# Performance work log

Measured on AMD Instinct MI355X. Metric: run time of the kernel, lower is better.

The kernel has to match this reference:

```python
import jax, jax.numpy as jnp
import numpy as np

B, T, IN_DIM = 128, 4096, 13
UNITS, MOTOR = 64, 6
LAYERS = [35, 23, 6]   # AutoNCP(64, 6): inter / command / motor neurons
_SPLITS = [35, 58]     # cumulative layer boundaries inside the 64-unit state


def setup_inputs() -> dict:
    keys = iter(jax.random.split(jax.random.key(0), 64))
    def rn(shape, s=0.1):
        return jax.random.normal(next(keys), shape, dtype=jnp.float32) * s
    inp = {"x": jax.random.normal(next(keys), (B, T, IN_DIM), dtype=jnp.float32)}
    # mixed-memory LSTM cell (ncps: input_map has bias, recurrent_map does not)
    inp["lstm_wi"] = rn((4 * UNITS, IN_DIM))
    inp["lstm_wh"] = rn((4 * UNITS, UNITS))
    inp["lstm_b"] = rn((4 * UNITS,))
    # wired CfC layers: ff1/ff2/time_a/time_b acting on concat([input, h])
    in_dims = [IN_DIM] + LAYERS[:-1]
    for i, (d, h) in enumerate(zip(in_dims, LAYERS)):
        for nm in ("w1", "w2", "wa", "wb"):
            inp[f"cfc{i}_{nm}"] = rn((h, d + h))
        for nm in ("b1", "b2", "ba", "bb"):
            inp[f"cfc{i}_{nm}"] = rn((h,))
    inp["gyro_w1"] = rn((32, MOTOR)); inp["gyro_b1"] = rn((32,))
    inp["gyro_w2"] = rn((3, 32));     inp["gyro_b2"] = rn((3,))
    inp["acc_w1"] = rn((32, MOTOR));  inp["acc_b1"] = rn((32,))
    inp["acc_w2"] = rn((3, 32));      inp["acc_b2"] = rn((3,))
    inp["unc_w1"] = rn((16, MOTOR));  inp["unc_b1"] = rn((16,))
    inp["unc_w2"] = rn((6, 16));      inp["unc_b2"] = rn((6,))
    return inp


def _cfc_step(inp, h, p):
    """ncps CfCCell, mode='default', no backbone, ts = 1.0."""
    W1, b1, W2, b2, Wa, ba, Wb, bb = p
    z = jnp.concatenate([inp, h], axis=-1)            # (B, in+hid)
    ff1 = jnp.tanh(z @ W1.T + b1)
    ff2 = jnp.tanh(z @ W2.T + b2)
    t = jax.nn.sigmoid((z @ Wa.T + ba) + (z @ Wb.T + bb))  # t_a*ts + t_b, ts==1
    return ff1 * (1.0 - t) + t * ff2


def reference(x, lstm_wi, lstm_wh, lstm_b,
              cfc0_w1, cfc0_b1, cfc0_w2, cfc0_b2, cfc0_wa, cfc0_ba, cfc0_wb, cfc0_bb,
              cfc1_w1, cfc1_b1, cfc1_w2, cfc1_b2, cfc1_wa, cfc1_ba, cfc1_wb, cfc1_bb,
              cfc2_w1, cfc2_b1, cfc2_w2, cfc2_b2, cfc2_wa, cfc2_ba, cfc2_wb, cfc2_bb,
              gyro_w1, gyro_b1, gyro_w2, gyro_b2,
              acc_w1, acc_b1, acc_w2, acc_b2,
              unc_w1, unc_b1, unc_w2, unc_b2):
    layer_params = (
        (cfc0_w1, cfc0_b1, cfc0_w2, cfc0_b2, cfc0_wa, cfc0_ba, cfc0_wb, cfc0_bb),
        (cfc1_w1, cfc1_b1, cfc1_w2, cfc1_b2, cfc1_wa, cfc1_ba, cfc1_wb, cfc1_bb),
        (cfc2_w1, cfc2_b1, cfc2_w2, cfc2_b2, cfc2_wa, cfc2_ba, cfc2_wb, cfc2_bb),
    )

    def step(carry, xt):  # xt: (B, 13)
        h, c = carry
        # mixed-memory LSTM over the full 64-unit state (forget gate +1.0)
        zg = xt @ lstm_wi.T + lstm_b + h @ lstm_wh.T
        ia, ig, fg, og = jnp.split(zg, 4, axis=-1)
        c_new = c * jax.nn.sigmoid(fg + 1.0) + jnp.tanh(ia) * jax.nn.sigmoid(ig)
        h_lstm = jnp.tanh(c_new) * jax.nn.sigmoid(og)
        # wired CfC: inter -> command -> motor, each fed previous layer's output
        hs = jnp.split(h_lstm, _SPLITS, axis=-1)
        inp = xt
        new_hs = []
        for hi, p in zip(hs, layer_params):
            inp = _cfc_step(inp, hi, p)
            new_hs.append(inp)
        return (jnp.concatenate(new_hs, axis=-1), c_new), inp  # motor out (B,6)

    Bsz = x.shape[0]
    h0 = jnp.zeros((Bsz, UNITS), x.dtype)
    c0 = jnp.zeros((Bsz, UNITS), x.dtype)
    _, outs = jax.lax.scan(step, (h0, c0), jnp.swapaxes(x, 0, 1))
    cfc_out = jnp.swapaxes(outs, 0, 1)  # (B, T, 6)

    gyro = jnp.tanh(cfc_out @ gyro_w1.T + gyro_b1) @ gyro_w2.T + gyro_b2
    acc = jnp.tanh(cfc_out @ acc_w1.T + acc_b1) @ acc_w2.T + acc_b2
    pred = jnp.concatenate([gyro, acc], axis=-1)                      # (B, T, 6)
    unc = jax.nn.softplus(
        jax.nn.relu(cfc_out @ unc_w1.T + unc_b1) @ unc_w2.T + unc_b2)  # (B, T, 6)
    return pred, unc
```

## Files before the change

### kernel.cpp

```cpp
#include <hip/hip_runtime.h>
#include <math.h>

#define BATCH 128
#define TSTEPS 4096
#define INDIM 13
#define XT 64


__device__ __forceinline__ float fsig(float x) {
    return __builtin_amdgcn_rcpf(1.f + __expf(-x));
}
__device__ __forceinline__ float ftanh(float x) {
    float s = fsig(x + x);
    return s + s - 1.f;
}
__device__ __forceinline__ float fsoftplus(float x) {
    return (x > 15.f) ? x : __logf(1.f + __expf(x));
}

__device__ __forceinline__ float qxor1(float v) {
    return __int_as_float(__builtin_amdgcn_update_dpp(
        0, __float_as_int(v), 0xB1, 0xF, 0xF, true));
}
__device__ __forceinline__ float qxor2(float v) {
    return __int_as_float(__builtin_amdgcn_update_dpp(
        0, __float_as_int(v), 0x4E, 0xF, 0xF, true));
}
__device__ __forceinline__ float hmir(float v) {
    return __int_as_float(__builtin_amdgcn_update_dpp(
        0, __float_as_int(v), 0x141, 0xF, 0xF, true));
}
#define BFLY8(a) { a += qxor1(a); a += qxor2(a); a += hmir(a); }

#define FMA4(acc, W, q, zv) { acc += zv.x * W##_##q##_0; acc += zv.y * W##_##q##_1; \
                              acc += zv.z * W##_##q##_2; acc += zv.w * W##_##q##_3; }

__global__ __launch_bounds__(512, 2)
void rnn_kernel(const float* __restrict__ x,
                const float* __restrict__ lstm_wi, const float* __restrict__ lstm_wh,
                const float* __restrict__ lstm_b,
                const float* __restrict__ c0w1, const float* __restrict__ c0w2,
                const float* __restrict__ c0wa, const float* __restrict__ c0wb,
                const float* __restrict__ c0b1, const float* __restrict__ c0b2,
                const float* __restrict__ c0ba, const float* __restrict__ c0bb,
                const float* __restrict__ c1w1, const float* __restrict__ c1w2,
                const float* __restrict__ c1wa, const float* __restrict__ c1wb,
                const float* __restrict__ c1b1, const float* __restrict__ c1b2,
                const float* __restrict__ c1ba, const float* __restrict__ c1bb,
                const float* __restrict__ c2w1, const float* __restrict__ c2w2,
                const float* __restrict__ c2wa, const float* __restrict__ c2wb,
                const float* __restrict__ c2b1, const float* __restrict__ c2b2,
                const float* __restrict__ c2ba, const float* __restrict__ c2bb,
                float* __restrict__ out)
{
    const int bb = blockIdx.x;
    const int t  = threadIdx.x;
    const int k  = t & 7;
    const int u  = t >> 3;

    __shared__ __align__(16) float smem[2688];
    float* zL  = smem;
    float* z0  = smem + 96;
    float* z1  = smem + 160;
    float* z2  = smem + 224;
    float* xt0 = smem + 256;
    float* xt1 = smem + 1088;
    float* ot0 = smem + 1920;
    float* ot1 = smem + 2304;

    const long xbase = (long)bb * TSTEPS * INDIM;
    const long obase = (long)bb * TSTEPS * 6;

    auto lwf = [&](int A, int c) -> float {
        int r = A * 64 + u;
        return (c < 13) ? lstm_wi[r * 13 + c]
             : (c < 77) ? lstm_wh[r * 64 + (c - 13)] : 0.f;
    };
#define DEF_WL(A,q) \
    float wl##A##_##q##_0 = lwf(A, 12*k + 4*q + 0); \
    float wl##A##_##q##_1 = lwf(A, 12*k + 4*q + 1); \
    float wl##A##_##q##_2 = lwf(A, 12*k + 4*q + 2); \
    float wl##A##_##q##_3 = lwf(A, 12*k + 4*q + 3);
    DEF_WL(0,0) DEF_WL(0,1) DEF_WL(0,2)
    DEF_WL(1,0) DEF_WL(1,1) DEF_WL(1,2)
    DEF_WL(2,0) DEF_WL(2,1) DEF_WL(2,2)
    DEF_WL(3,0) DEF_WL(3,1) DEF_WL(3,2)
#undef DEF_WL
    const float bL0 = lstm_b[u];
    const float bL1 = lstm_b[64 + u];
    const float bL2 = lstm_b[128 + u];
    const float bL3 = lstm_b[192 + u];

    const int grp  = (u < 35) ? 0 : (u < 58) ? 1 : 2;
    const int row  = (grp == 0) ? u : (grp == 1) ? (u - 35) : (u - 58);
    const int rl   = (grp == 0) ? 48 : (grp == 1) ? 58 : 29;
    const int clen = (grp == 2) ? 4 : 8;
    const int cb   = (grp == 2) ? 4 * k : 8 * k;
    const float *W0p, *W1p, *W2p, *W3p;
    float bC0, bC1, bC2, bC3;
    if (grp == 0) {
        W0p = c0w1 + row * 48; W1p = c0w2 + row * 48;
        W2p = c0wa + row * 48; W3p = c0wb + row * 48;
        bC0 = c0b1[row]; bC1 = c0b2[row]; bC2 = c0ba[row]; bC3 = c0bb[row];
    } else if (grp == 1) {
        W0p = c1w1 + row * 58; W1p = c1w2 + row * 58;
        W2p = c1wa + row * 58; W3p = c1wb + row * 58;
        bC0 = c1b1[row]; bC1 = c1b2[row]; bC2 = c1ba[row]; bC3 = c1bb[row];
    } else {
        W0p = c2w1 + row * 29; W1p = c2w2 + row * 29;
        W2p = c2wa + row * 29; W3p = c2wb + row * 29;
        bC0 = c2b1[row]; bC1 = c2b2[row]; bC2 = c2ba[row]; bC3 = c2bb[row];
    }
    auto cwf = [&](const float* W, int c) -> float {
        int cc = cb + c;
        return (c < clen && cc < rl) ? W[cc] : 0.f;
    };
#define DEF_WC(A,q) \
    float wc##A##_##q##_0 = cwf(W##A##p, 4*q + 0); \
    float wc##A##_##q##_1 = cwf(W##A##p, 4*q + 1); \
    float wc##A##_##q##_2 = cwf(W##A##p, 4*q + 2); \
    float wc##A##_##q##_3 = cwf(W##A##p, 4*q + 3);
    DEF_WC(0,0) DEF_WC(0,1)
    DEF_WC(1,0) DEF_WC(1,1)
    DEF_WC(2,0) DEF_WC(2,1)
    DEF_WC(3,0) DEF_WC(3,1)
#undef DEF_WC

    float creg = 0.f;

    if (t < 256) smem[t] = 0.f;
    if (t < 208) {
        float4 xi = *(const float4*)(x + xbase + 4 * t);
        *(float4*)&xt0[4 * t] = xi;
    }
    if (t < 13) zL[t] = x[xbase + t];
    __syncthreads();

    #pragma unroll 1
    for (int ts = 0; ts < TSTEPS; ++ts) {
        const int par = (ts >> 6) & 1;
        const int lts = ts & 63;

        if (t >= 256 && t < 269) z0[t - 256] = zL[t - 256];
        {
            const float4* zc = (const float4*)(zL + 12 * k);
            float4 q0 = zc[0], q1 = zc[1], q2 = zc[2];
            float a0 = 0.f, a1 = 0.f, a2 = 0.f, a3 = 0.f;
            FMA4(a0, wl0, 0, q0) FMA4(a0, wl0, 1, q1) FMA4(a0, wl0, 2, q2)
            FMA4(a1, wl1, 0, q0) FMA4(a1, wl1, 1, q1) FMA4(a1, wl1, 2, q2)
            FMA4(a2, wl2, 0, q0) FMA4(a2, wl2, 1, q1) FMA4(a2, wl2, 2, q2)
            FMA4(a3, wl3, 0, q0) FMA4(a3, wl3, 1, q1) FMA4(a3, wl3, 2, q2)
            BFLY8(a0) BFLY8(a1) BFLY8(a2) BFLY8(a3)
            a0 += bL0; a1 += bL1; a2 += bL2; a3 += bL3;
            float cn = creg * fsig(a2 + 1.f) + ftanh(a0) * fsig(a1);
            creg = cn;
            float hl = ftanh(cn) * fsig(a3);
            if (k == 0) {
                if (u < 35)      z0[13 + u] = hl;
                else if (u < 58) z1[u]      = hl;
                else             z2[u - 35] = hl;
            }
        }
        __syncthreads();

        if (grp == 0) {
            const float4* zc = (const float4*)(z0 + 8 * k);
            float4 v0 = zc[0], v1 = zc[1];
            float a0 = 0.f, a1 = 0.f, a2 = 0.f, a3 = 0.f;
            FMA4(a0, wc0, 0, v0) FMA4(a0, wc0, 1, v1)
            FMA4(a1, wc1, 0, v0) FMA4(a1, wc1, 1, v1)
            FMA4(a2, wc2, 0, v0) FMA4(a2, wc2, 1, v1)
            FMA4(a3, wc3, 0, v0) FMA4(a3, wc3, 1, v1)
            BFLY8(a0) BFLY8(a1) BFLY8(a2) BFLY8(a3)
            a0 += bC0; a1 += bC1; a2 += bC2; a3 += bC3;
            float tg = fsig(a2 + a3);
            float f1 = ftanh(a0), f2 = ftanh(a1);
            float o = f1 + tg * (f2 - f1);
            if (k == 0) { z1[row] = o; zL[13 + row] = o; }
        } else {
            if (lts == 62 && (ts + 2) < TSTEPS) {
                int i = t - 280;
                if (i < 208) {
                    float4 v = *(const float4*)(x + xbase + (long)(ts + 2) * 13 + 4 * i);
                    float* dst = par ? xt0 : xt1;
                    *(float4*)&dst[4 * i] = v;
                }
            }
            if (lts == 0 && ts > 0) {
                int i = t - 280;
                if (i < 96) {
                    const float* src = par ? ot0 : ot1;
                    float4 v = *(const float4*)&src[4 * i];
                    *(float4*)(out + obase + (long)(ts - XT) * 6 + 4 * i) = v;
                }
            }
        }
        __syncthreads();

        if (grp == 1) {
            const float4* zc = (const float4*)(z1 + 8 * k);
            float4 v0 = zc[0], v1 = zc[1];
            float a0 = 0.f, a1 = 0.f, a2 = 0.f, a3 = 0.f;
            FMA4(a0, wc0, 0, v0) FMA4(a0, wc0, 1, v1)
            FMA4(a1, wc1, 0, v0) FMA4(a1, wc1, 1, v1)
            FMA4(a2, wc2, 0, v0) FMA4(a2, wc2, 1, v1)
            FMA4(a3, wc3, 0, v0) FMA4(a3, wc3, 1, v1)
            BFLY8(a0) BFLY8(a1) BFLY8(a2) BFLY8(a3)
            a0 += bC0; a1 += bC1; a2 += bC2; a3 += bC3;
            float tg = fsig(a2 + a3);
            float f1 = ftanh(a0), f2 = ftanh(a1);
            float o = f1 + tg * (f2 - f1);
            if (k == 0) { z2[row] = o; zL[48 + row] = o; }
        }
        __syncthreads();

        if (grp == 2) {
            const float4* zc = (const float4*)(z2 + 4 * k);
            float4 v0 = zc[0];
            float a0 = 0.f, a1 = 0.f, a2 = 0.f, a3 = 0.f;
            FMA4(a0, wc0, 0, v0)
            FMA4(a1, wc1, 0, v0)
            FMA4(a2, wc2, 0, v0)
            FMA4(a3, wc3, 0, v0)
            BFLY8(a0) BFLY8(a1) BFLY8(a2) BFLY8(a3)
            a0 += bC0; a1 += bC1; a2 += bC2; a3 += bC3;
            float tg = fsig(a2 + a3);
            float f1 = ftanh(a0), f2 = ftanh(a1);
            float o = f1 + tg * (f2 - f1);
            if (k == 0) {
                zL[71 + row] = o;
                float* ob = par ? ot1 : ot0;
                ob[lts * 6 + row] = o;
            }
        } else if (t < 13 && (ts + 1) < TSTEPS) {
            const float* xb = (((ts + 1) >> 6) & 1) ? xt1 : xt0;
            zL[t] = xb[((ts + 1) & 63) * 13 + t];
        }
        __syncthreads();
    }

    {
        int i = t - 280;
        if (i >= 0 && i < 96) {
            float4 v = *(const float4*)&ot1[4 * i];
            *(float4*)(out + obase + (long)(TSTEPS - XT) * 6 + 4 * i) = v;
        }
    }
}

#define S_GW1 0
#define S_GB1 192
#define S_GW2 224
#define S_GB2 320
#define S_AW1 323
#define S_AB1 515
#define S_AW2 547
#define S_AB2 643
#define S_UW1 646
#define S_UB1 742
#define S_UW2 758
#define S_UB2 854
#define S_TOT 860

__global__ __launch_bounds__(256)
void head_kernel(const float* __restrict__ gw1, const float* __restrict__ gb1,
                 const float* __restrict__ gw2, const float* __restrict__ gb2,
                 const float* __restrict__ aw1, const float* __restrict__ ab1,
                 const float* __restrict__ aw2, const float* __restrict__ ab2,
                 const float* __restrict__ uw1, const float* __restrict__ ub1,
                 const float* __restrict__ uw2, const float* __restrict__ ub2,
                 float* __restrict__ out)
{
    __shared__ float s[S_TOT];
    const int t = threadIdx.x;
    if (t < 192) { s[S_GW1 + t] = gw1[t]; s[S_AW1 + t] = aw1[t]; }
    if (t < 96)  { s[S_GW2 + t] = gw2[t]; s[S_AW2 + t] = aw2[t];
                   s[S_UW1 + t] = uw1[t]; s[S_UW2 + t] = uw2[t]; }
    if (t < 32)  { s[S_GB1 + t] = gb1[t]; s[S_AB1 + t] = ab1[t]; }
    if (t < 16)  { s[S_UB1 + t] = ub1[t]; }
    if (t < 3)   { s[S_GB2 + t] = gb2[t]; s[S_AB2 + t] = ab2[t]; }
    if (t < 6)   { s[S_UB2 + t] = ub2[t]; }
    __syncthreads();

    const long p = (long)blockIdx.x * 256 + t;
    const long base = p * 6;
    float m0 = out[base+0], m1 = out[base+1], m2 = out[base+2];
    float m3 = out[base+3], m4 = out[base+4], m5 = out[base+5];

    float gy0 = s[S_GB2+0], gy1 = s[S_GB2+1], gy2 = s[S_GB2+2];
    float ac0 = s[S_AB2+0], ac1 = s[S_AB2+1], ac2 = s[S_AB2+2];
    #pragma unroll
    for (int i = 0; i < 32; ++i) {
        float hg = s[S_GB1+i] + s[S_GW1+i*6+0]*m0 + s[S_GW1+i*6+1]*m1
                 + s[S_GW1+i*6+2]*m2 + s[S_GW1+i*6+3]*m3
                 + s[S_GW1+i*6+4]*m4 + s[S_GW1+i*6+5]*m5;
        hg = ftanh(hg);
        gy0 += s[S_GW2+i]*hg; gy1 += s[S_GW2+32+i]*hg; gy2 += s[S_GW2+64+i]*hg;
        float ha = s[S_AB1+i] + s[S_AW1+i*6+0]*m0 + s[S_AW1+i*6+1]*m1
                 + s[S_AW1+i*6+2]*m2 + s[S_AW1+i*6+3]*m3
                 + s[S_AW1+i*6+4]*m4 + s[S_AW1+i*6+5]*m5;
        ha = ftanh(ha);
        ac0 += s[S_AW2+i]*ha; ac1 += s[S_AW2+32+i]*ha; ac2 += s[S_AW2+64+i]*ha;
    }
    float u0 = s[S_UB2+0], u1 = s[S_UB2+1], u2 = s[S_UB2+2];
    float u3 = s[S_UB2+3], u4 = s[S_UB2+4], u5 = s[S_UB2+5];
    #pragma unroll
    for (int i = 0; i < 16; ++i) {
        float hu = s[S_UB1+i] + s[S_UW1+i*6+0]*m0 + s[S_UW1+i*6+1]*m1
                 + s[S_UW1+i*6+2]*m2 + s[S_UW1+i*6+3]*m3
                 + s[S_UW1+i*6+4]*m4 + s[S_UW1+i*6+5]*m5;
        hu = fmaxf(hu, 0.f);
        u0 += s[S_UW2+i]*hu;      u1 += s[S_UW2+16+i]*hu; u2 += s[S_UW2+32+i]*hu;
        u3 += s[S_UW2+48+i]*hu;   u4 += s[S_UW2+64+i]*hu; u5 += s[S_UW2+80+i]*hu;
    }
    out[base+0] = gy0; out[base+1] = gy1; out[base+2] = gy2;
    out[base+3] = ac0; out[base+4] = ac1; out[base+5] = ac2;
    const long uoff = (long)BATCH * TSTEPS * 6;
    out[uoff+base+0] = fsoftplus(u0); out[uoff+base+1] = fsoftplus(u1);
    out[uoff+base+2] = fsoftplus(u2); out[uoff+base+3] = fsoftplus(u3);
    out[uoff+base+4] = fsoftplus(u4); out[uoff+base+5] = fsoftplus(u5);
}

extern "C" void kernel_launch(void* const* d_in, const int* in_sizes, int n_in,
                              void* d_out, int out_size, void* d_ws, size_t ws_size,
                              hipStream_t stream) {
    const float* x       = (const float*)d_in[0];
    const float* lstm_wi = (const float*)d_in[1];
    const float* lstm_wh = (const float*)d_in[2];
    const float* lstm_b  = (const float*)d_in[3];
    const float* c0w1 = (const float*)d_in[4];
    const float* c0w2 = (const float*)d_in[5];
    const float* c0wa = (const float*)d_in[6];
    const float* c0wb = (const float*)d_in[7];
    const float* c0b1 = (const float*)d_in[8];
    const float* c0b2 = (const float*)d_in[9];
    const float* c0ba = (const float*)d_in[10];
    const float* c0bb = (const float*)d_in[11];
    const float* c1w1 = (const float*)d_in[12];
    const float* c1w2 = (const float*)d_in[13];
    const float* c1wa = (const float*)d_in[14];
    const float* c1wb = (const float*)d_in[15];
    const float* c1b1 = (const float*)d_in[16];
    const float* c1b2 = (const float*)d_in[17];
    const float* c1ba = (const float*)d_in[18];
    const float* c1bb = (const float*)d_in[19];
    const float* c2w1 = (const float*)d_in[20];
    const float* c2w2 = (const float*)d_in[21];
    const float* c2wa = (const float*)d_in[22];
    const float* c2wb = (const float*)d_in[23];
    const float* c2b1 = (const float*)d_in[24];
    const float* c2b2 = (const float*)d_in[25];
    const float* c2ba = (const float*)d_in[26];
    const float* c2bb = (const float*)d_in[27];
    const float* gw1 = (const float*)d_in[28];
    const float* gb1 = (const float*)d_in[29];
    const float* gw2 = (const float*)d_in[30];
    const float* gb2 = (const float*)d_in[31];
    const float* aw1 = (const float*)d_in[32];
    const float* ab1 = (const float*)d_in[33];
    const float* aw2 = (const float*)d_in[34];
    const float* ab2 = (const float*)d_in[35];
    const float* uw1 = (const float*)d_in[36];
    const float* ub1 = (const float*)d_in[37];
    const float* uw2 = (const float*)d_in[38];
    const float* ub2 = (const float*)d_in[39];
    float* out = (float*)d_out;

    rnn_kernel<<<BATCH, 512, 0, stream>>>(x, lstm_wi, lstm_wh, lstm_b,
        c0w1, c0w2, c0wa, c0wb, c0b1, c0b2, c0ba, c0bb,
        c1w1, c1w2, c1wa, c1wb, c1b1, c1b2, c1ba, c1bb,
        c2w1, c2w2, c2wa, c2wb, c2b1, c2b2, c2ba, c2bb, out);

    head_kernel<<<(BATCH * TSTEPS) / 256, 256, 0, stream>>>(
        gw1, gb1, gw2, gb2, aw1, ab1, aw2, ab2, uw1, ub1, uw2, ub2, out);
}
```

Measured before the change: 5.453 ms.

## Halve block to 256 threads with 4 lanes per unit and 2-step reductions

Each hidden unit's dot products now use 4 lanes instead of 8. Each lane holds twice as many weights in registers, and the cross-lane reduction drops from three DPP steps to two. The block shrinks from 512 to 256 threads (4 wavefronts instead of 8), which makes the per-step __syncthreads barriers cheaper. The x-tile prefetch and output copy are remapped to the new thread ranges. The step that copied zL into z0 is folded into the input load. The cost is more serial FMAs per lane and more register pressure.

```diff
diff --git a/kernel.cpp b/kernel.cpp
--- a/kernel.cpp
+++ b/kernel.cpp
@@ -26,16 +26,12 @@
     return __int_as_float(__builtin_amdgcn_update_dpp(
         0, __float_as_int(v), 0x4E, 0xF, 0xF, true));
 }
-__device__ __forceinline__ float hmir(float v) {
-    return __int_as_float(__builtin_amdgcn_update_dpp(
-        0, __float_as_int(v), 0x141, 0xF, 0xF, true));
-}
-#define BFLY8(a) { a += qxor1(a); a += qxor2(a); a += hmir(a); }
+#define BFLY4(a) { a += qxor1(a); a += qxor2(a); }
 
 #define FMA4(acc, W, q, zv) { acc += zv.x * W##_##q##_0; acc += zv.y * W##_##q##_1; \
                               acc += zv.z * W##_##q##_2; acc += zv.w * W##_##q##_3; }
 
-__global__ __launch_bounds__(512, 2)
+__global__ __launch_bounds__(256, 1)
 void rnn_kernel(const float* __restrict__ x,
                 const float* __restrict__ lstm_wi, const float* __restrict__ lstm_wh,
                 const float* __restrict__ lstm_b,
@@ -55,8 +51,8 @@
 {
     const int bb = blockIdx.x;
     const int t  = threadIdx.x;
-    const int k  = t & 7;
-    const int u  = t >> 3;
+    const int k  = t & 3;
+    const int u  = t >> 2;
 
     __shared__ __align__(16) float smem[2688];
     float* zL  = smem;
@@ -77,14 +73,14 @@
              : (c < 77) ? lstm_wh[r * 64 + (c - 13)] : 0.f;
     };
 #define DEF_WL(A,q) \
-    float wl##A##_##q##_0 = lwf(A, 12*k + 4*q + 0); \
-    float wl##A##_##q##_1 = lwf(A, 12*k + 4*q + 1); \
-    float wl##A##_##q##_2 = lwf(A, 12*k + 4*q + 2); \
-    float wl##A##_##q##_3 = lwf(A, 12*k + 4*q + 3);
-    DEF_WL(0,0) DEF_WL(0,1) DEF_WL(0,2)
-    DEF_WL(1,0) DEF_WL(1,1) DEF_WL(1,2)
-    DEF_WL(2,0) DEF_WL(2,1) DEF_WL(2,2)
-    DEF_WL(3,0) DEF_WL(3,1) DEF_WL(3,2)
+    float wl##A##_##q##_0 = lwf(A, 24*k + 4*q + 0); \
+    float wl##A##_##q##_1 = lwf(A, 24*k + 4*q + 1); \
+    float wl##A##_##q##_2 = lwf(A, 24*k + 4*q + 2); \
+    float wl##A##_##q##_3 = lwf(A, 24*k + 4*q + 3);
+    DEF_WL(0,0) DEF_WL(0,1) DEF_WL(0,2) DEF_WL(0,3) DEF_WL(0,4) DEF_WL(0,5)
+    DEF_WL(1,0) DEF_WL(1,1) DEF_WL(1,2) DEF_WL(1,3) DEF_WL(1,4) DEF_WL(1,5)
+    DEF_WL(2,0) DEF_WL(2,1) DEF_WL(2,2) DEF_WL(2,3) DEF_WL(2,4) DEF_WL(2,5)
+    DEF_WL(3,0) DEF_WL(3,1) DEF_WL(3,2) DEF_WL(3,3) DEF_WL(3,4) DEF_WL(3,5)
 #undef DEF_WL
     const float bL0 = lstm_b[u];
     const float bL1 = lstm_b[64 + u];
@@ -94,8 +90,8 @@
     const int grp  = (u < 35) ? 0 : (u < 58) ? 1 : 2;
     const int row  = (grp == 0) ? u : (grp == 1) ? (u - 35) : (u - 58);
     const int rl   = (grp == 0) ? 48 : (grp == 1) ? 58 : 29;
-    const int clen = (grp == 2) ? 4 : 8;
-    const int cb   = (grp == 2) ? 4 * k : 8 * k;
+    const int clen = (grp == 0) ? 12 : (grp == 1) ? 16 : 8;
+    const int cb   = clen * k;
     const float *W0p, *W1p, *W2p, *W3p;
     float bC0, bC1, bC2, bC3;
     if (grp == 0) {
@@ -120,20 +116,20 @@
     float wc##A##_##q##_1 = cwf(W##A##p, 4*q + 1); \
     float wc##A##_##q##_2 = cwf(W##A##p, 4*q + 2); \
     float wc##A##_##q##_3 = cwf(W##A##p, 4*q + 3);
-    DEF_WC(0,0) DEF_WC(0,1)
-    DEF_WC(1,0) DEF_WC(1,1)
-    DEF_WC(2,0) DEF_WC(2,1)
-    DEF_WC(3,0) DEF_WC(3,1)
+    DEF_WC(0,0) DEF_WC(0,1) DEF_WC(0,2) DEF_WC(0,3)
+    DEF_WC(1,0) DEF_WC(1,1) DEF_WC(1,2) DEF_WC(1,3)
+    DEF_WC(2,0) DEF_WC(2,1) DEF_WC(2,2) DEF_WC(2,3)
+    DEF_WC(3,0) DEF_WC(3,1) DEF_WC(3,2) DEF_WC(3,3)
 #undef DEF_WC
 
     float creg = 0.f;
 
-    if (t < 256) smem[t] = 0.f;
+    smem[t] = 0.f;
     if (t < 208) {
         float4 xi = *(const float4*)(x + xbase + 4 * t);
         *(float4*)&xt0[4 * t] = xi;
     }
-    if (t < 13) zL[t] = x[xbase + t];
+    if (t < 13) { float x0 = x[xbase + t]; zL[t] = x0; z0[t] = x0; }
     __syncthreads();
 
     #pragma unroll 1
@@ -141,16 +137,20 @@
         const int par = (ts >> 6) & 1;
         const int lts = ts & 63;
 
-        if (t >= 256 && t < 269) z0[t - 256] = zL[t - 256];
         {
-            const float4* zc = (const float4*)(zL + 12 * k);
-            float4 q0 = zc[0], q1 = zc[1], q2 = zc[2];
+            const float4* zc = (const float4*)(zL + 24 * k);
+            float4 q0 = zc[0], q1 = zc[1], q2 = zc[2],
+                   q3 = zc[3], q4 = zc[4], q5 = zc[5];
             float a0 = 0.f, a1 = 0.f, a2 = 0.f, a3 = 0.f;
             FMA4(a0, wl0, 0, q0) FMA4(a0, wl0, 1, q1) FMA4(a0, wl0, 2, q2)
+            FMA4(a0, wl0, 3, q3) FMA4(a0, wl0, 4, q4) FMA4(a0, wl0, 5, q5)
             FMA4(a1, wl1, 0, q0) FMA4(a1, wl1, 1, q1) FMA4(a1, wl1, 2, q2)
+            FMA4(a1, wl1, 3, q3) FMA4(a1, wl1, 4, q4) FMA4(a1, wl1, 5, q5)
             FMA4(a2, wl2, 0, q0) FMA4(a2, wl2, 1, q1) FMA4(a2, wl2, 2, q2)
+            FMA4(a2, wl2, 3, q3) FMA4(a2, wl2, 4, q4) FMA4(a2, wl2, 5, q5)
             FMA4(a3, wl3, 0, q0) FMA4(a3, wl3, 1, q1) FMA4(a3, wl3, 2, q2)
-            BFLY8(a0) BFLY8(a1) BFLY8(a2) BFLY8(a3)
+            FMA4(a3, wl3, 3, q3) FMA4(a3, wl3, 4, q4) FMA4(a3, wl3, 5, q5)
+            BFLY4(a0) BFLY4(a1) BFLY4(a2) BFLY4(a3)
             a0 += bL0; a1 += bL1; a2 += bL2; a3 += bL3;
             float cn = creg * fsig(a2 + 1.f) + ftanh(a0) * fsig(a1);
             creg = cn;
@@ -164,14 +164,14 @@
         __syncthreads();
 
         if (grp == 0) {
-            const float4* zc = (const float4*)(z0 + 8 * k);
-            float4 v0 = zc[0], v1 = zc[1];
+            const float4* zc = (const float4*)(z0 + 12 * k);
+            float4 v0 = zc[0], v1 = zc[1], v2 = zc[2];
             float a0 = 0.f, a1 = 0.f, a2 = 0.f, a3 = 0.f;
-            FMA4(a0, wc0, 0, v0) FMA4(a0, wc0, 1, v1)
-            FMA4(a1, wc1, 0, v0) FMA4(a1, wc1, 1, v1)
-            FMA4(a2, wc2, 0, v0) FMA4(a2, wc2, 1, v1)
-            FMA4(a3, wc3, 0, v0) FMA4(a3, wc3, 1, v1)
-            BFLY8(a0) BFLY8(a1) BFLY8(a2) BFLY8(a3)
+            FMA4(a0, wc0, 0, v0) FMA4(a0, wc0, 1, v1) FMA4(a0, wc0, 2, v2)
+            FMA4(a1, wc1, 0, v0) FMA4(a1, wc1, 1, v1) FMA4(a1, wc1, 2, v2)
+            FMA4(a2, wc2, 0, v0) FMA4(a2, wc2, 1, v1) FMA4(a2, wc2, 2, v2)
+            FMA4(a3, wc3, 0, v0) FMA4(a3, wc3, 1, v1) FMA4(a3, wc3, 2, v2)
+            BFLY4(a0) BFLY4(a1) BFLY4(a2) BFLY4(a3)
             a0 += bC0; a1 += bC1; a2 += bC2; a3 += bC3;
             float tg = fsig(a2 + a3);
             float f1 = ftanh(a0), f2 = ftanh(a1);
@@ -179,15 +179,14 @@
             if (k == 0) { z1[row] = o; zL[13 + row] = o; }
         } else {
             if (lts == 62 && (ts + 2) < TSTEPS) {
-                int i = t - 280;
-                if (i < 208) {
-                    float4 v = *(const float4*)(x + xbase + (long)(ts + 2) * 13 + 4 * i);
-                    float* dst = par ? xt0 : xt1;
-                    *(float4*)&dst[4 * i] = v;
-                }
+                int i = (t - 140) * 2;
+                float* dst = par ? xt0 : xt1;
+                const float* src = x + xbase + (long)(ts + 2) * 13;
+                if (i < 208)     *(float4*)&dst[4*i]     = *(const float4*)(src + 4*i);
+                if (i + 1 < 208) *(float4*)&dst[4*(i+1)] = *(const float4*)(src + 4*(i+1));
             }
             if (lts == 0 && ts > 0) {
-                int i = t - 280;
+                int i = t - 140;
                 if (i < 96) {
                     const float* src = par ? ot0 : ot1;
                     float4 v = *(const float4*)&src[4 * i];
@@ -198,14 +197,14 @@
         __syncthreads();
 
         if (grp == 1) {
-            const float4* zc = (const float4*)(z1 + 8 * k);
-            float4 v0 = zc[0], v1 = zc[1];
+            const float4* zc = (const float4*)(z1 + 16 * k);
+            float4 v0 = zc[0], v1 = zc[1], v2 = zc[2], v3 = zc[3];
             float a0 = 0.f, a1 = 0.f, a2 = 0.f, a3 = 0.f;
-            FMA4(a0, wc0, 0, v0) FMA4(a0, wc0, 1, v1)
-            FMA4(a1, wc1, 0, v0) FMA4(a1, wc1, 1, v1)
-            FMA4(a2, wc2, 0, v0) FMA4(a2, wc2, 1, v1)
-            FMA4(a3, wc3, 0, v0) FMA4(a3, wc3, 1, v1)
-            BFLY8(a0) BFLY8(a1) BFLY8(a2) BFLY8(a3)
+            FMA4(a0, wc0, 0, v0) FMA4(a0, wc0, 1, v1) FMA4(a0, wc0, 2, v2) FMA4(a0, wc0, 3, v3)
+            FMA4(a1, wc1, 0, v0) FMA4(a1, wc1, 1, v1) FMA4(a1, wc1, 2, v2) FMA4(a1, wc1, 3, v3)
+            FMA4(a2, wc2, 0, v0) FMA4(a2, wc2, 1, v1) FMA4(a2, wc2, 2, v2) FMA4(a2, wc2, 3, v3)
+            FMA4(a3, wc3, 0, v0) FMA4(a3, wc3, 1, v1) FMA4(a3, wc3, 2, v2) FMA4(a3, wc3, 3, v3)
+            BFLY4(a0) BFLY4(a1) BFLY4(a2) BFLY4(a3)
             a0 += bC0; a1 += bC1; a2 += bC2; a3 += bC3;
             float tg = fsig(a2 + a3);
             float f1 = ftanh(a0), f2 = ftanh(a1);
@@ -215,14 +214,14 @@
         __syncthreads();
 
         if (grp == 2) {
-            const float4* zc = (const float4*)(z2 + 4 * k);
-            float4 v0 = zc[0];
+            const float4* zc = (const float4*)(z2 + 8 * k);
+            float4 v0 = zc[0], v1 = zc[1];
             float a0 = 0.f, a1 = 0.f, a2 = 0.f, a3 = 0.f;
-            FMA4(a0, wc0, 0, v0)
-            FMA4(a1, wc1, 0, v0)
-            FMA4(a2, wc2, 0, v0)
-            FMA4(a3, wc3, 0, v0)
-            BFLY8(a0) BFLY8(a1) BFLY8(a2) BFLY8(a3)
+            FMA4(a0, wc0, 0, v0) FMA4(a0, wc0, 1, v1)
+            FMA4(a1, wc1, 0, v0) FMA4(a1, wc1, 1, v1)
+            FMA4(a2, wc2, 0, v0) FMA4(a2, wc2, 1, v1)
+            FMA4(a3, wc3, 0, v0) FMA4(a3, wc3, 1, v1)
+            BFLY4(a0) BFLY4(a1) BFLY4(a2) BFLY4(a3)
             a0 += bC0; a1 += bC1; a2 += bC2; a3 += bC3;
             float tg = fsig(a2 + a3);
             float f1 = ftanh(a0), f2 = ftanh(a1);
@@ -234,17 +233,15 @@
             }
         } else if (t < 13 && (ts + 1) < TSTEPS) {
             const float* xb = (((ts + 1) >> 6) & 1) ? xt1 : xt0;
-            zL[t] = xb[((ts + 1) & 63) * 13 + t];
+            float xn = xb[((ts + 1) & 63) * 13 + t];
+            zL[t] = xn; z0[t] = xn;
         }
         __syncthreads();
     }
 
-    {
-        int i = t - 280;
-        if (i >= 0 && i < 96) {
-            float4 v = *(const float4*)&ot1[4 * i];
-            *(float4*)(out + obase + (long)(TSTEPS - XT) * 6 + 4 * i) = v;
-        }
+    if (t < 96) {
+        float4 v = *(const float4*)&ot1[4 * t];
+        *(float4*)(out + obase + (long)(TSTEPS - XT) * 6 + 4 * t) = v;
     }
 }
 
@@ -366,7 +363,7 @@
     const float* ub2 = (const float*)d_in[39];
     float* out = (float*)d_out;
 
-    rnn_kernel<<<BATCH, 512, 0, stream>>>(x, lstm_wi, lstm_wh, lstm_b,
+    rnn_kernel<<<BATCH, 256, 0, stream>>>(x, lstm_wi, lstm_wh, lstm_b,
         c0w1, c0w2, c0wa, c0wb, c0b1, c0b2, c0ba, c0bb,
         c1w1, c1w2, c1wa, c1wb, c1b1, c1b2, c1ba, c1bb,
         c2w1, c2w2, c2wa, c2wb, c2b1, c2b2, c2ba, c2bb, out);
```

Result: faster. 5.323 ms (-2.4%).
